# Kernel optimization log

Hardware: AMD Instinct MI355X
Metric: run time of the kernel (lower is better)

## Reference

```python
import jax, jax.numpy as jnp
import numpy as np

N_INST, N_PERS, N_PROD = 20000, 50000, 30000
E_INST, E_PERS, E_PROD = 160000, 400000, 240000
F_IN, HID, HEADS, OUT = 128, 64, 4, 2
D = HID * HEADS  # 256
NEG_SLOPE_ATT = 0.2   # GATv2 attention leaky-relu slope
NEG_SLOPE_ACT = 0.01  # F.leaky_relu default
BN_EPS = 1e-5


def gatv2(x, src, dst, Wl, Wr, att, b, N):
    """Single-relation GATv2Conv (concat heads, add_self_loops=True)."""
    loop = jnp.arange(N, dtype=src.dtype)
    s = jnp.concatenate([src, loop])
    d = jnp.concatenate([dst, loop])
    H, C = att.shape
    hl = (x @ Wl).reshape(N, H, C)  # source transform
    hr = (x @ Wr).reshape(N, H, C)  # target transform
    e = jax.nn.leaky_relu(hl[s] + hr[d], NEG_SLOPE_ATT)        # [E,H,C]
    score = jnp.einsum('ehc,hc->eh', e, att)                   # [E,H]
    mx = jax.lax.stop_gradient(jax.ops.segment_max(score, d, num_segments=N))
    ex = jnp.exp(score - mx[d])
    den = jax.ops.segment_sum(ex, d, num_segments=N)           # [N,H]
    alpha = ex / (den[d] + 1e-16)
    out = jax.ops.segment_sum(alpha[..., None] * hl[s], d, num_segments=N)
    return out.reshape(N, H * C) + b


def batchnorm(x, g, b):
    mu = jnp.mean(x, axis=0)
    var = jnp.var(x, axis=0)
    return (x - mu) * jax.lax.rsqrt(var + BN_EPS) * g + b


def setup_inputs() -> dict:
    key = jax.random.key(0)
    ks = jax.random.split(key, 16)
    s = 0.05
    return {
        'x_inst': jax.random.normal(ks[0], (N_INST, F_IN), jnp.float32),
        'x_pers': jax.random.normal(ks[1], (N_PERS, F_IN), jnp.float32),
        'x_prod': jax.random.normal(ks[2], (N_PROD, F_IN), jnp.float32),
        'ei_inst': jax.random.randint(ks[3], (2, E_INST), 0, N_INST, jnp.int32),
        'ei_pers': jax.random.randint(ks[4], (2, E_PERS), 0, N_PERS, jnp.int32),
        'ei_prod': jax.random.randint(ks[5], (2, E_PROD), 0, N_PROD, jnp.int32),
        'Wl1': jax.random.normal(ks[6], (3, F_IN, D), jnp.float32) * s,
        'Wr1': jax.random.normal(ks[7], (3, F_IN, D), jnp.float32) * s,
        'att1': jax.random.normal(ks[8], (3, HEADS, HID), jnp.float32) * s,
        'b1': jnp.zeros((3, D), jnp.float32),
        'Wl2': jax.random.normal(ks[9], (3, D, D), jnp.float32) * s,
        'Wr2': jax.random.normal(ks[10], (3, D, D), jnp.float32) * s,
        'att2': jax.random.normal(ks[11], (3, HEADS, HID), jnp.float32) * s,
        'b2': jnp.zeros((3, D), jnp.float32),
        'bn_g': jnp.ones((3, D), jnp.float32),
        'bn_b': jnp.zeros((3, D), jnp.float32),
        'cW': jax.random.normal(ks[12], (D, OUT), jnp.float32) * s,
        'cb': jnp.zeros((OUT,), jnp.float32),
    }


def reference(x_inst, x_pers, x_prod, ei_inst, ei_pers, ei_prod,
              Wl1, Wr1, att1, b1, Wl2, Wr2, att2, b2,
              bn_g, bn_b, cW, cb):
    xs = (x_inst, x_pers, x_prod)
    eis = (ei_inst, ei_pers, ei_prod)
    outs = []
    for i in range(3):  # fixed set of node types
        x = xs[i]
        N = x.shape[0]
        src, dst = eis[i][0], eis[i][1]
        h = gatv2(x, src, dst, Wl1[i], Wr1[i], att1[i], b1[i], N)
        h = jax.nn.leaky_relu(batchnorm(h, bn_g[i], bn_b[i]), NEG_SLOPE_ACT)
        h = gatv2(h, src, dst, Wl2[i], Wr2[i], att2[i], b2[i], N)
        h = jax.nn.leaky_relu(batchnorm(h, bn_g[i], bn_b[i]), NEG_SLOPE_ACT)
        outs.append(h @ cW + cb)
    return tuple(outs)
```

## Files before the change

### kernel.cpp

```cpp
#include <hip/hip_runtime.h>

#define DFEAT 256
#define NEG_ATT 0.2f
#define NEG_ACT 0.01f
#define BN_EPS 1e-5f

typedef short bf16x8 __attribute__((ext_vector_type(8)));
typedef float f32x4 __attribute__((ext_vector_type(4)));

struct Int3 { int a[3]; };
struct Cp3 { const void* p[3]; };
struct Vp3 { void* p[3]; };
struct WJobs { const float* src[12]; unsigned short* dst[12]; int K[12]; };

__device__ __forceinline__ float lrelu(float x, float s) { return x > 0.f ? x : s * x; }

__device__ __forceinline__ unsigned short f2bf(float f) {
    union { float f; unsigned int u; } v; v.f = f;
    unsigned int u = v.u;
    unsigned int r = (u + 0x7FFFu + ((u >> 16) & 1u)) >> 16;
    return (unsigned short)r;
}
__device__ __forceinline__ float bf2f(unsigned short s) {
    union { unsigned int u; float f; } v; v.u = ((unsigned int)s) << 16;
    return v.f;
}
__device__ __forceinline__ float u_lo(unsigned u) {
    union { unsigned u; float f; } v; v.u = u << 16; return v.f;
}
__device__ __forceinline__ float u_hi(unsigned u) {
    union { unsigned u; float f; } v; v.u = u & 0xffff0000u; return v.f;
}

__global__ __launch_bounds__(256)
void hist_all_k(Cp3 dst, Int3 E, int* __restrict__ counts_all, Int3 nodeOff) {
    int t = blockIdx.y;
    int e = blockIdx.x * 256 + threadIdx.x;
    if (e >= E.a[t]) return;
    const int* dstp = (const int*)dst.p[t];
    atomicAdd(&counts_all[nodeOff.a[t] + dstp[e]], 1);
}

__global__ __launch_bounds__(256)
void scan1_all_k(const int* __restrict__ counts_all, int* __restrict__ offs_all,
                 int* __restrict__ bsums_all, Int3 N, Int3 nodeOff, Int3 bOff) {
    int t = blockIdx.y;
    if (blockIdx.x * 256 >= N.a[t]) return;
    const int* counts = counts_all + nodeOff.a[t];
    int* offs = offs_all + nodeOff.a[t] + t;
    int* bsums = bsums_all + bOff.a[t];
    __shared__ int buf[256];
    int tt = threadIdx.x;
    int i = blockIdx.x * 256 + tt;
    int v = (i < N.a[t]) ? counts[i] : 0;
    buf[tt] = v;
    __syncthreads();
    for (int off = 1; off < 256; off <<= 1) {
        int x = (tt >= off) ? buf[tt - off] : 0;
        __syncthreads();
        buf[tt] += x;
        __syncthreads();
    }
    if (i < N.a[t]) offs[i] = buf[tt];
    if (tt == 255) bsums[blockIdx.x] = buf[255];
}

__global__ __launch_bounds__(256)
void scan2_all_k(int* __restrict__ bsums_all, Int3 N, Int3 bOff) {
    int t = blockIdx.x;
    int nb = (N.a[t] + 255) / 256;
    int* bsums = bsums_all + bOff.a[t];
    __shared__ int buf[256];
    __shared__ int carry_s;
    int tt = threadIdx.x;
    if (tt == 0) carry_s = 0;
    __syncthreads();
    for (int base = 0; base < nb; base += 256) {
        int i = base + tt;
        int v = (i < nb) ? bsums[i] : 0;
        buf[tt] = v;
        __syncthreads();
        for (int off = 1; off < 256; off <<= 1) {
            int x = (tt >= off) ? buf[tt - off] : 0;
            __syncthreads();
            buf[tt] += x;
            __syncthreads();
        }
        int incl = buf[tt];
        int c = carry_s;
        if (i < nb) bsums[i] = c + incl - v;
        __syncthreads();
        if (tt == 255) carry_s = c + buf[255];
        __syncthreads();
    }
}

__global__ __launch_bounds__(256)
void scan3_all_k(int* __restrict__ offs_all, const int* __restrict__ counts_all,
                 const int* __restrict__ bsums_all, Int3 N, Int3 E,
                 Int3 nodeOff, Int3 bOff) {
    int t = blockIdx.y;
    if (blockIdx.x * 256 >= N.a[t]) return;
    int* offs = offs_all + nodeOff.a[t] + t;
    const int* counts = counts_all + nodeOff.a[t];
    const int* bsums = bsums_all + bOff.a[t];
    int i = blockIdx.x * 256 + threadIdx.x;
    if (i < N.a[t]) offs[i] = offs[i] - counts[i] + bsums[blockIdx.x];
    if (i == 0) offs[N.a[t]] = E.a[t];
}

__global__ __launch_bounds__(256)
void scatter_all_k(Cp3 src, Cp3 dst, Int3 E, const int* __restrict__ offs_all,
                   int* __restrict__ counts_all, int* __restrict__ csr_all,
                   Int3 nodeOff, Int3 edgeOff) {
    int t = blockIdx.y;
    int e = blockIdx.x * 256 + threadIdx.x;
    if (e >= E.a[t]) return;
    const int* srcp = (const int*)src.p[t];
    const int* dstp = (const int*)dst.p[t];
    const int* offs = offs_all + nodeOff.a[t] + t;
    int* cursor = counts_all + nodeOff.a[t];
    int* csr = csr_all + edgeOff.a[t];
    int d = dstp[e];
    int pos = atomicSub(&cursor[d], 1) - 1;
    csr[offs[d] + pos] = srcp[e];
}

__global__ __launch_bounds__(256)
void wcast_tr_k(WJobs jobs) {
    int j = blockIdx.z;
    int K = jobs.K[j];
    int k0 = blockIdx.y * 64;
    if (k0 >= K) return;
    int n0 = blockIdx.x * 64;
    const float* W = jobs.src[j];
    unsigned short* Bt = jobs.dst[j];
    __shared__ float tile[64][65];
    int tid = threadIdx.x;
    int tr = tid >> 4;
    int tc4 = (tid & 15) << 2;
#pragma unroll
    for (int r = 0; r < 4; ++r) {
        int k = tr + r * 16;
        float4 v = *(const float4*)(W + (size_t)(k0 + k) * 256 + n0 + tc4);
        tile[k][tc4] = v.x; tile[k][tc4 + 1] = v.y;
        tile[k][tc4 + 2] = v.z; tile[k][tc4 + 3] = v.w;
    }
    __syncthreads();
    int n = tid >> 2;
    int kc = (tid & 3) << 4;
    unsigned o[8];
#pragma unroll
    for (int q = 0; q < 8; ++q) {
        float v0 = tile[kc + 2 * q][n];
        float v1 = tile[kc + 2 * q + 1][n];
        o[q] = (unsigned)f2bf(v0) | ((unsigned)f2bf(v1) << 16);
    }
    unsigned short* dp = Bt + (size_t)(n0 + n) * K + k0 + kc;
    *(uint4*)dp = make_uint4(o[0], o[1], o[2], o[3]);
    *(uint4*)(dp + 8) = make_uint4(o[4], o[5], o[6], o[7]);
}

template<int AMODE>
__global__ __launch_bounds__(256)
void mfma_gemm_all_k(Cp3 Ap3, Cp3 Bp3, Cp3 ssP, Vp3 Cp3v, Int3 M3, int K) {
    int t = blockIdx.z;
    int M = M3.a[t];
    int bm = blockIdx.x * 128;
    if (bm >= M) return;
    const void* Ap = Ap3.p[t];
    const unsigned short* Bt = (const unsigned short*)Bp3.p[t];
    const float* ss = (const float*)ssP.p[t];
    unsigned short* C = (unsigned short*)Cp3v.p[t];
    const int LDK = 40;
    __shared__ unsigned short As[128 * LDK];
    __shared__ unsigned short Bs[128 * LDK];
    int tid = threadIdx.x;
    int bn = blockIdx.y * 128;
    int wid = tid >> 6, lane = tid & 63;
    int quad = lane >> 4, l16 = lane & 15;
    int mw = (wid & 1) * 64, nw = (wid >> 1) * 64;
    f32x4 acc[4][4] = {};
    for (int k0 = 0; k0 < K; k0 += 32) {
#pragma unroll
        for (int i = 0; i < 2; ++i) {
            int c = tid + 256 * i;
            int row = c >> 2, ko = (c & 3) * 8;
            int ra = bm + row; if (ra >= M) ra = M - 1;
            if (AMODE == 1) {
                const float* Af = (const float*)Ap;
                float4 a0 = *(const float4*)(Af + (size_t)ra * K + k0 + ko);
                float4 a1 = *(const float4*)(Af + (size_t)ra * K + k0 + ko + 4);
                ushort4 lo, hi;
                lo.x = f2bf(a0.x); lo.y = f2bf(a0.y); lo.z = f2bf(a0.z); lo.w = f2bf(a0.w);
                hi.x = f2bf(a1.x); hi.y = f2bf(a1.y); hi.z = f2bf(a1.z); hi.w = f2bf(a1.w);
                *(ushort4*)&As[row * LDK + ko] = lo;
                *(ushort4*)&As[row * LDK + ko + 4] = hi;
            } else if (AMODE == 2) {
                const unsigned short* Ab = (const unsigned short*)Ap;
                uint4 va = *(const uint4*)(Ab + (size_t)ra * K + k0 + ko);
                const unsigned* up = (const unsigned*)&va;
                float4 sc0 = *(const float4*)(ss + k0 + ko);
                float4 sc1 = *(const float4*)(ss + k0 + ko + 4);
                float4 sh0 = *(const float4*)(ss + 256 + k0 + ko);
                float4 sh1 = *(const float4*)(ss + 256 + k0 + ko + 4);
                float fv[8] = {u_lo(up[0]), u_hi(up[0]), u_lo(up[1]), u_hi(up[1]),
                               u_lo(up[2]), u_hi(up[2]), u_lo(up[3]), u_hi(up[3])};
                float scv[8] = {sc0.x, sc0.y, sc0.z, sc0.w, sc1.x, sc1.y, sc1.z, sc1.w};
                float shv[8] = {sh0.x, sh0.y, sh0.z, sh0.w, sh1.x, sh1.y, sh1.z, sh1.w};
                unsigned ov[4];
#pragma unroll
                for (int q = 0; q < 4; ++q) {
                    float v0 = fmaf(fv[2 * q], scv[2 * q], shv[2 * q]);
                    v0 = fmaxf(v0, NEG_ACT * v0);
                    float v1 = fmaf(fv[2 * q + 1], scv[2 * q + 1], shv[2 * q + 1]);
                    v1 = fmaxf(v1, NEG_ACT * v1);
                    ov[q] = (unsigned)f2bf(v0) | ((unsigned)f2bf(v1) << 16);
                }
                *(uint4*)&As[row * LDK + ko] = make_uint4(ov[0], ov[1], ov[2], ov[3]);
            } else {
                const unsigned short* Ab = (const unsigned short*)Ap;
                uint4 va = *(const uint4*)(Ab + (size_t)ra * K + k0 + ko);
                *(uint4*)&As[row * LDK + ko] = va;
            }
            uint4 vb = *(const uint4*)(Bt + (size_t)(bn + row) * K + k0 + ko);
            *(uint4*)&Bs[row * LDK + ko] = vb;
        }
        __syncthreads();
        bf16x8 af[4], bfv[4];
#pragma unroll
        for (int i = 0; i < 4; ++i)
            af[i] = *(bf16x8*)&As[(mw + 16 * i + l16) * LDK + quad * 8];
#pragma unroll
        for (int u = 0; u < 4; ++u)
            bfv[u] = *(bf16x8*)&Bs[(nw + 16 * u + l16) * LDK + quad * 8];
#pragma unroll
        for (int i = 0; i < 4; ++i)
#pragma unroll
            for (int u = 0; u < 4; ++u)
                acc[i][u] = __builtin_amdgcn_mfma_f32_16x16x32_bf16(af[i], bfv[u], acc[i][u], 0, 0, 0);
        __syncthreads();
    }
#pragma unroll
    for (int i = 0; i < 4; ++i) {
#pragma unroll
        for (int r = 0; r < 4; ++r) {
            int grow = bm + mw + 16 * i + quad * 4 + r;
            if (grow < M) {
#pragma unroll
                for (int u = 0; u < 4; ++u) {
                    int gcol = bn + nw + 16 * u + l16;
                    C[(size_t)grow * 512 + gcol] = f2bf(acc[i][u][r]);
                }
            }
        }
    }
}

__global__ __launch_bounds__(256)
void gat_gather_all_k(Cp3 hl3, Cp3 offs3, Cp3 csr3, Cp3 att3, Cp3 bias3,
                      Vp3 out3, Int3 N3) {
    int t = blockIdx.z;
    int N = N3.a[t];
    int wave = (blockIdx.x * 256 + threadIdx.x) >> 6;
    int lane = threadIdx.x & 63;
    if (wave >= N) return;
    const char* hlB = (const char*)hl3.p[t];
    const int* offs = (const int*)offs3.p[t];
    const int* csr = (const int*)csr3.p[t];
    const float* att = (const float*)att3.p[t];
    const float* bias = (const float*)bias3.p[t];
    unsigned short* out = (unsigned short*)out3.p[t];
    int d = wave;
    unsigned lOff = (unsigned)lane << 3;
    ushort4 hru = *(const ushort4*)(hlB + (((unsigned)d << 10) + 512u + lOff));
    float hr0 = bf2f(hru.x), hr1 = bf2f(hru.y), hr2 = bf2f(hru.z), hr3 = bf2f(hru.w);
    float4 av  = *(const float4*)(att + (lane << 2));
    float4 bv  = *(const float4*)(bias + (lane << 2));
    float l = 0.f, ac0 = 0.f, ac1 = 0.f, ac2 = 0.f, ac3 = 0.f;

    auto update = [&](ushort4 u) {
        float h0 = bf2f(u.x), h1 = bf2f(u.y), h2 = bf2f(u.z), h3 = bf2f(u.w);
        float x0 = h0 + hr0; x0 = fmaxf(x0, NEG_ATT * x0);
        float x1 = h1 + hr1; x1 = fmaxf(x1, NEG_ATT * x1);
        float x2 = h2 + hr2; x2 = fmaxf(x2, NEG_ATT * x2);
        float x3 = h3 + hr3; x3 = fmaxf(x3, NEG_ATT * x3);
        float part = x0 * av.x;
        part = fmaf(x1, av.y, part);
        part = fmaf(x2, av.z, part);
        part = fmaf(x3, av.w, part);
        part += __shfl_xor(part, 1);
        part += __shfl_xor(part, 2);
        part += __shfl_xor(part, 4);
        part += __shfl_xor(part, 8);
        float p = __expf(part);
        l += p;
        ac0 = fmaf(p, h0, ac0); ac1 = fmaf(p, h1, ac1);
        ac2 = fmaf(p, h2, ac2); ac3 = fmaf(p, h3, ac3);
    };

    update(*(const ushort4*)(hlB + (((unsigned)d << 10) + lOff)));

    int beg = offs[d];
    int deg = offs[d + 1] - beg;
    for (int base = 0; base < deg; base += 64) {
        int cnt = min(64, deg - base);
        int my = (base + lane < deg) ? csr[beg + base + lane] : d;
        for (int j = 0; j < cnt; j += 8) {
            int kk = min(8, cnt - j);
            ushort4 v[8];
#pragma unroll
            for (int u = 0; u < 8; ++u) {
                int s = __shfl(my, (j + u) & 63);
                if (u < kk) v[u] = *(const ushort4*)(hlB + (((unsigned)s << 10) + lOff));
            }
#pragma unroll
            for (int u = 0; u < 8; ++u)
                if (u < kk) update(v[u]);
        }
    }
    float inv = 1.f / (l + 1e-16f);
    ushort4 o;
    o.x = f2bf(fmaf(ac0, inv, bv.x));
    o.y = f2bf(fmaf(ac1, inv, bv.y));
    o.z = f2bf(fmaf(ac2, inv, bv.z));
    o.w = f2bf(fmaf(ac3, inv, bv.w));
    *(ushort4*)((char*)out + (((unsigned)d << 9) + lOff)) = o;
}

__global__ __launch_bounds__(256)
void bn_stats_all_k(Cp3 h3, Vp3 st3, Int3 N3) {
    int t = blockIdx.y;
    const unsigned short* hp = (const unsigned short*)h3.p[t];
    float* st = (float*)st3.p[t];
    long total = (long)N3.a[t] * 256;
    int tid = threadIdx.x;
    long gt = (long)blockIdx.x * 256 + tid;
    long stride = (long)gridDim.x * 256 * 8;
    float s[8] = {0.f}, s2[8] = {0.f};
    for (long p = gt * 8; p < total; p += stride) {
        uint4 u = *(const uint4*)(hp + p);
        unsigned short* us = (unsigned short*)&u;
#pragma unroll
        for (int j = 0; j < 8; ++j) { float v = bf2f(us[j]); s[j] += v; s2[j] += v * v; }
    }
#pragma unroll
    for (int j = 0; j < 8; ++j) { s[j] += __shfl_xor(s[j], 32); s2[j] += __shfl_xor(s2[j], 32); }
    __shared__ float lds[2048];
    int wv = tid >> 6, lane = tid & 63;
    if (lane < 32) {
#pragma unroll
        for (int j = 0; j < 8; ++j) {
            lds[wv * 512 + lane * 8 + j] = s[j];
            lds[wv * 512 + 256 + lane * 8 + j] = s2[j];
        }
    }
    __syncthreads();
    for (int q = tid; q < 512; q += 256) {
        float v = lds[q] + lds[512 + q] + lds[1024 + q] + lds[1536 + q];
        atomicAdd(&st[q], v);
    }
}

__global__ __launch_bounds__(256)
void bn_finalize_all_k(Cp3 st3, const float* __restrict__ gb, const float* __restrict__ bb,
                       Vp3 ss3, Int3 N3) {
    int t = blockIdx.x;
    const float* st = (const float*)st3.p[t];
    float* ss = (float*)ss3.p[t];
    int f = threadIdx.x;
    float invN = 1.f / (float)N3.a[t];
    float mu  = st[f] * invN;
    float var = st[256 + f] * invN - mu * mu;
    float sc  = gb[t * DFEAT + f] / sqrtf(var + BN_EPS);
    ss[f] = sc;
    ss[256 + f] = bb[t * DFEAT + f] - mu * sc;
}

__global__ __launch_bounds__(256)
void bn_cls_all_k(Cp3 R3, Cp3 st3, const float* __restrict__ gb, const float* __restrict__ bb,
                  const float* __restrict__ cW, const float* __restrict__ cb,
                  Vp3 out3, Int3 N3) {
    int t = blockIdx.y;
    int N = N3.a[t];
    int wave = (blockIdx.x * 256 + threadIdx.x) >> 6;
    int lane = threadIdx.x & 63;
    if (wave >= N) return;
    const unsigned short* R = (const unsigned short*)R3.p[t];
    const float* stats = (const float*)st3.p[t];
    const float* g = gb + (size_t)t * DFEAT;
    const float* b = bb + (size_t)t * DFEAT;
    float* out = (float*)out3.p[t];
    int f4 = lane << 2;
    float invN = 1.f / (float)N;
    ushort4 u = *(const ushort4*)(R + (size_t)wave * DFEAT + f4);
    float vv[4] = {bf2f(u.x), bf2f(u.y), bf2f(u.z), bf2f(u.w)};
    float p0 = 0.f, p1 = 0.f;
#pragma unroll
    for (int j = 0; j < 4; ++j) {
        int f = f4 + j;
        float mu  = stats[f] * invN;
        float var = stats[DFEAT + f] * invN - mu * mu;
        float sc  = g[f] / sqrtf(var + BN_EPS);
        float val = lrelu((vv[j] - mu) * sc + b[f], NEG_ACT);
        float2 w = *(const float2*)(cW + (size_t)f * 2);
        p0 += val * w.x;
        p1 += val * w.y;
    }
#pragma unroll
    for (int off = 1; off < 64; off <<= 1) {
        p0 += __shfl_xor(p0, off);
        p1 += __shfl_xor(p1, off);
    }
    if (lane == 0) {
        out[(size_t)wave * 2 + 0] = p0 + cb[0];
        out[(size_t)wave * 2 + 1] = p1 + cb[1];
    }
}

extern "C" void kernel_launch(void* const* d_in, const int* in_sizes, int n_in,
                              void* d_out, int out_size, void* d_ws, size_t ws_size,
                              hipStream_t stream) {
    const float* x0 = (const float*)d_in[0];
    const float* x1 = (const float*)d_in[1];
    const float* x2 = (const float*)d_in[2];
    const int* ei[3] = {(const int*)d_in[3], (const int*)d_in[4], (const int*)d_in[5]};
    const float* Wl1 = (const float*)d_in[6];
    const float* Wr1 = (const float*)d_in[7];
    const float* att1 = (const float*)d_in[8];
    const float* b1 = (const float*)d_in[9];
    const float* Wl2 = (const float*)d_in[10];
    const float* Wr2 = (const float*)d_in[11];
    const float* att2 = (const float*)d_in[12];
    const float* b2 = (const float*)d_in[13];
    const float* bn_g = (const float*)d_in[14];
    const float* bn_b = (const float*)d_in[15];
    const float* cW = (const float*)d_in[16];
    const float* cb = (const float*)d_in[17];

    Int3 N3, E3, nodeOff, edgeOff, bOff;
    N3.a[0] = in_sizes[0] / 128; N3.a[1] = in_sizes[1] / 128; N3.a[2] = in_sizes[2] / 128;
    E3.a[0] = in_sizes[3] / 2;   E3.a[1] = in_sizes[4] / 2;   E3.a[2] = in_sizes[5] / 2;
    int Ntot = 0, Etot = 0, btot = 0;
    int maxN = 0, maxE = 0;
    for (int i = 0; i < 3; ++i) {
        nodeOff.a[i] = Ntot; edgeOff.a[i] = Etot; bOff.a[i] = btot;
        Ntot += N3.a[i]; Etot += E3.a[i]; btot += (N3.a[i] + 255) / 256;
        if (N3.a[i] > maxN) maxN = N3.a[i];
        if (E3.a[i] > maxE) maxE = E3.a[i];
    }

    char* w = (char*)d_ws;
    auto alloc_b = [&](size_t bytes) -> void* {
        void* p = (void*)w;
        w += (bytes + 255) & ~(size_t)255;
        return p;
    };
    unsigned short* C_all  = (unsigned short*)alloc_b((size_t)Ntot * 512 * sizeof(unsigned short));
    unsigned short* Rb_all = (unsigned short*)alloc_b((size_t)Ntot * DFEAT * sizeof(unsigned short));
    unsigned short* Bt1 = (unsigned short*)alloc_b((size_t)3 * 512 * 128 * sizeof(unsigned short));
    unsigned short* Bt2 = (unsigned short*)alloc_b((size_t)3 * 512 * 256 * sizeof(unsigned short));
    int* counts_all = (int*)alloc_b((size_t)Ntot * sizeof(int));
    int* offs_all   = (int*)alloc_b((size_t)(Ntot + 3) * sizeof(int));
    int* csr_all    = (int*)alloc_b((size_t)Etot * sizeof(int));
    int* bsums_all  = (int*)alloc_b((size_t)btot * sizeof(int));
    float* stats_all = (float*)alloc_b((size_t)6 * 512 * sizeof(float));
    float* ss_all    = (float*)alloc_b((size_t)3 * 512 * sizeof(float));

    Cp3 srcP, dstP, xP, Bt1P, Bt2P, hlP, offsP, csrP, att1P, att2P, b1P, b2P;
    Cp3 RbCP, st1CP, st2CP, ssCP, dumP;
    Vp3 CP, RbP, st1P, st2P, ssP, outP;
    for (int i = 0; i < 3; ++i) {
        srcP.p[i] = ei[i];
        dstP.p[i] = ei[i] + E3.a[i];
        xP.p[i] = (i == 0) ? (const void*)x0 : (i == 1) ? (const void*)x1 : (const void*)x2;
        Bt1P.p[i] = Bt1 + (size_t)i * 512 * 128;
        Bt2P.p[i] = Bt2 + (size_t)i * 512 * 256;
        CP.p[i] = C_all + (size_t)nodeOff.a[i] * 512;
        hlP.p[i] = CP.p[i];
        RbP.p[i] = Rb_all + (size_t)nodeOff.a[i] * DFEAT;
        RbCP.p[i] = RbP.p[i];
        offsP.p[i] = offs_all + nodeOff.a[i] + i;
        csrP.p[i] = csr_all + edgeOff.a[i];
        att1P.p[i] = att1 + (size_t)i * DFEAT;
        att2P.p[i] = att2 + (size_t)i * DFEAT;
        b1P.p[i] = b1 + (size_t)i * DFEAT;
        b2P.p[i] = b2 + (size_t)i * DFEAT;
        st1P.p[i] = stats_all + (size_t)i * 512;
        st2P.p[i] = stats_all + (size_t)(3 + i) * 512;
        st1CP.p[i] = st1P.p[i];
        st2CP.p[i] = st2P.p[i];
        ssP.p[i] = ss_all + (size_t)i * 512;
        ssCP.p[i] = ssP.p[i];
        dumP.p[i] = xP.p[i];
        outP.p[i] = (float*)d_out + (size_t)nodeOff.a[i] * 2;
    }

    int maxNblk = (maxN + 255) / 256;
    int maxEblk = (maxE + 255) / 256;
    int maxMtile = (maxN + 127) / 128;
    int maxNwave = (maxN + 3) / 4;

    hipMemsetAsync(counts_all, 0, (size_t)Ntot * sizeof(int), stream);
    hipMemsetAsync(stats_all, 0, (size_t)6 * 512 * sizeof(float), stream);
    {
        WJobs jobs;
        for (int i = 0; i < 3; ++i) {
            jobs.src[i * 4 + 0] = Wl1 + (size_t)i * 128 * 256;
            jobs.dst[i * 4 + 0] = (unsigned short*)Bt1P.p[i];
            jobs.K[i * 4 + 0] = 128;
            jobs.src[i * 4 + 1] = Wr1 + (size_t)i * 128 * 256;
            jobs.dst[i * 4 + 1] = (unsigned short*)Bt1P.p[i] + (size_t)256 * 128;
            jobs.K[i * 4 + 1] = 128;
            jobs.src[i * 4 + 2] = Wl2 + (size_t)i * 256 * 256;
            jobs.dst[i * 4 + 2] = (unsigned short*)Bt2P.p[i];
            jobs.K[i * 4 + 2] = 256;
            jobs.src[i * 4 + 3] = Wr2 + (size_t)i * 256 * 256;
            jobs.dst[i * 4 + 3] = (unsigned short*)Bt2P.p[i] + (size_t)256 * 256;
            jobs.K[i * 4 + 3] = 256;
        }
        wcast_tr_k<<<dim3(4, 4, 12), 256, 0, stream>>>(jobs);
    }

    hist_all_k<<<dim3(maxEblk, 3), 256, 0, stream>>>(dstP, E3, counts_all, nodeOff);
    scan1_all_k<<<dim3(maxNblk, 3), 256, 0, stream>>>(counts_all, offs_all, bsums_all, N3, nodeOff, bOff);
    scan2_all_k<<<3, 256, 0, stream>>>(bsums_all, N3, bOff);
    scan3_all_k<<<dim3(maxNblk, 3), 256, 0, stream>>>(offs_all, counts_all, bsums_all, N3, E3, nodeOff, bOff);
    scatter_all_k<<<dim3(maxEblk, 3), 256, 0, stream>>>(srcP, dstP, E3, offs_all, counts_all, csr_all, nodeOff, edgeOff);

    mfma_gemm_all_k<1><<<dim3(maxMtile, 4, 3), 256, 0, stream>>>(xP, Bt1P, dumP, CP, N3, 128);
    gat_gather_all_k<<<dim3(maxNwave, 1, 3), 256, 0, stream>>>(hlP, offsP, csrP, att1P, b1P, RbP, N3);
    bn_stats_all_k<<<dim3(512, 3), 256, 0, stream>>>(RbCP, st1P, N3);
    bn_finalize_all_k<<<3, 256, 0, stream>>>(st1CP, bn_g, bn_b, ssP, N3);

    mfma_gemm_all_k<2><<<dim3(maxMtile, 4, 3), 256, 0, stream>>>(RbCP, Bt2P, ssCP, CP, N3, 256);
    gat_gather_all_k<<<dim3(maxNwave, 1, 3), 256, 0, stream>>>(hlP, offsP, csrP, att2P, b2P, RbP, N3);
    bn_stats_all_k<<<dim3(512, 3), 256, 0, stream>>>(RbCP, st2P, N3);

    bn_cls_all_k<<<dim3(maxNwave, 3), 256, 0, stream>>>(RbCP, st2CP, bn_g, bn_b, cW, cb, outP, N3);
}
```

Measured before the change: 562.2 us.

## Fuse three-pass CSR scan into one block-per-type kernel and fold memsets into wcast

```diff
diff --git a/kernel.cpp b/kernel.cpp
--- a/kernel.cpp
+++ b/kernel.cpp
@@ -41,72 +41,63 @@
     atomicAdd(&counts_all[nodeOff.a[t] + dstp[e]], 1);
 }
 
-__global__ __launch_bounds__(256)
-void scan1_all_k(const int* __restrict__ counts_all, int* __restrict__ offs_all,
-                 int* __restrict__ bsums_all, Int3 N, Int3 nodeOff, Int3 bOff) {
-    int t = blockIdx.y;
-    if (blockIdx.x * 256 >= N.a[t]) return;
+__global__ __launch_bounds__(1024)
+void scan_fused_k(const int* __restrict__ counts_all, int* __restrict__ offs_all,
+                  Int3 N3, Int3 E3, Int3 nodeOff) {
+    int t = blockIdx.x;
+    int N = N3.a[t];
     const int* counts = counts_all + nodeOff.a[t];
     int* offs = offs_all + nodeOff.a[t] + t;
-    int* bsums = bsums_all + bOff.a[t];
-    __shared__ int buf[256];
-    int tt = threadIdx.x;
-    int i = blockIdx.x * 256 + tt;
-    int v = (i < N.a[t]) ? counts[i] : 0;
-    buf[tt] = v;
-    __syncthreads();
-    for (int off = 1; off < 256; off <<= 1) {
-        int x = (tt >= off) ? buf[tt - off] : 0;
+    __shared__ int ldsT[16];
+    __shared__ int ldsE[16];
+    __shared__ int ldsTot;
+    int tid = threadIdx.x;
+    int wv = tid >> 6, lane = tid & 63;
+    int carry = 0;
+    for (int base = 0; base < N; base += 8192) {
+        int idx0 = base + tid * 8;
+        int c[8];
+#pragma unroll
+        for (int j = 0; j < 8; ++j) {
+            int i = idx0 + j;
+            c[j] = (i < N) ? counts[i] : 0;
+        }
+        int tsum = 0;
+#pragma unroll
+        for (int j = 0; j < 8; ++j) tsum += c[j];
+        int incl = tsum;
+#pragma unroll
+        for (int off = 1; off < 64; off <<= 1) {
+            int v = __shfl_up(incl, off);
+            if (lane >= off) incl += v;
+        }
+        int texcl = incl - tsum;
+        if (lane == 63) ldsT[wv] = incl;
         __syncthreads();
-        buf[tt] += x;
+        if (wv == 0) {
+            int v = (lane < 16) ? ldsT[lane] : 0;
+            int inc2 = v;
+#pragma unroll
+            for (int off = 1; off < 16; off <<= 1) {
+                int u2 = __shfl_up(inc2, off);
+                if (lane >= off) inc2 += u2;
+            }
+            if (lane < 16) ldsE[lane] = inc2 - v;
+            if (lane == 15) ldsTot = inc2;
+        }
         __syncthreads();
-    }
-    if (i < N.a[t]) offs[i] = buf[tt];
-    if (tt == 255) bsums[blockIdx.x] = buf[255];
-}
-
-__global__ __launch_bounds__(256)
-void scan2_all_k(int* __restrict__ bsums_all, Int3 N, Int3 bOff) {
-    int t = blockIdx.x;
-    int nb = (N.a[t] + 255) / 256;
-    int* bsums = bsums_all + bOff.a[t];
-    __shared__ int buf[256];
-    __shared__ int carry_s;
-    int tt = threadIdx.x;
-    if (tt == 0) carry_s = 0;
-    __syncthreads();
-    for (int base = 0; base < nb; base += 256) {
-        int i = base + tt;
-        int v = (i < nb) ? bsums[i] : 0;
-        buf[tt] = v;
+        int mybase = carry + ldsE[wv] + texcl;
+        int pfx = 0;
+#pragma unroll
+        for (int j = 0; j < 8; ++j) {
+            int i = idx0 + j;
+            if (i < N) offs[i] = mybase + pfx;
+            pfx += c[j];
+        }
+        carry += ldsTot;
         __syncthreads();
-        for (int off = 1; off < 256; off <<= 1) {
-            int x = (tt >= off) ? buf[tt - off] : 0;
-            __syncthreads();
-            buf[tt] += x;
-            __syncthreads();
-        }
-        int incl = buf[tt];
-        int c = carry_s;
-        if (i < nb) bsums[i] = c + incl - v;
-        __syncthreads();
-        if (tt == 255) carry_s = c + buf[255];
-        __syncthreads();
-    }
-}
-
-__global__ __launch_bounds__(256)
-void scan3_all_k(int* __restrict__ offs_all, const int* __restrict__ counts_all,
-                 const int* __restrict__ bsums_all, Int3 N, Int3 E,
-                 Int3 nodeOff, Int3 bOff) {
-    int t = blockIdx.y;
-    if (blockIdx.x * 256 >= N.a[t]) return;
-    int* offs = offs_all + nodeOff.a[t] + t;
-    const int* counts = counts_all + nodeOff.a[t];
-    const int* bsums = bsums_all + bOff.a[t];
-    int i = blockIdx.x * 256 + threadIdx.x;
-    if (i < N.a[t]) offs[i] = offs[i] - counts[i] + bsums[blockIdx.x];
-    if (i == 0) offs[N.a[t]] = E.a[t];
+    }
+    if (tid == 0) offs[N] = E3.a[t];
 }
 
 __global__ __launch_bounds__(256)
@@ -127,7 +118,15 @@
 }
 
 __global__ __launch_bounds__(256)
-void wcast_tr_k(WJobs jobs) {
+void wcast_tr_k(WJobs jobs, int* __restrict__ counts_all, int Ntot,
+                float* __restrict__ stats_all) {
+    {
+        int bid = (blockIdx.z * gridDim.y + blockIdx.y) * gridDim.x + blockIdx.x;
+        int nthr = gridDim.x * gridDim.y * gridDim.z * 256;
+        int gtid = bid * 256 + threadIdx.x;
+        for (int i = gtid; i < Ntot; i += nthr) counts_all[i] = 0;
+        for (int i = gtid; i < 3072; i += nthr) stats_all[i] = 0.f;
+    }
     int j = blockIdx.z;
     int K = jobs.K[j];
     int k0 = blockIdx.y * 64;
@@ -438,14 +437,14 @@
     const float* cW = (const float*)d_in[16];
     const float* cb = (const float*)d_in[17];
 
-    Int3 N3, E3, nodeOff, edgeOff, bOff;
+    Int3 N3, E3, nodeOff, edgeOff;
     N3.a[0] = in_sizes[0] / 128; N3.a[1] = in_sizes[1] / 128; N3.a[2] = in_sizes[2] / 128;
     E3.a[0] = in_sizes[3] / 2;   E3.a[1] = in_sizes[4] / 2;   E3.a[2] = in_sizes[5] / 2;
-    int Ntot = 0, Etot = 0, btot = 0;
+    int Ntot = 0, Etot = 0;
     int maxN = 0, maxE = 0;
     for (int i = 0; i < 3; ++i) {
-        nodeOff.a[i] = Ntot; edgeOff.a[i] = Etot; bOff.a[i] = btot;
-        Ntot += N3.a[i]; Etot += E3.a[i]; btot += (N3.a[i] + 255) / 256;
+        nodeOff.a[i] = Ntot; edgeOff.a[i] = Etot;
+        Ntot += N3.a[i]; Etot += E3.a[i];
         if (N3.a[i] > maxN) maxN = N3.a[i];
         if (E3.a[i] > maxE) maxE = E3.a[i];
     }
@@ -463,7 +462,6 @@
     int* counts_all = (int*)alloc_b((size_t)Ntot * sizeof(int));
     int* offs_all   = (int*)alloc_b((size_t)(Ntot + 3) * sizeof(int));
     int* csr_all    = (int*)alloc_b((size_t)Etot * sizeof(int));
-    int* bsums_all  = (int*)alloc_b((size_t)btot * sizeof(int));
     float* stats_all = (float*)alloc_b((size_t)6 * 512 * sizeof(float));
     float* ss_all    = (float*)alloc_b((size_t)3 * 512 * sizeof(float));
 
@@ -496,13 +494,10 @@
         outP.p[i] = (float*)d_out + (size_t)nodeOff.a[i] * 2;
     }
 
-    int maxNblk = (maxN + 255) / 256;
     int maxEblk = (maxE + 255) / 256;
     int maxMtile = (maxN + 127) / 128;
     int maxNwave = (maxN + 3) / 4;
 
-    hipMemsetAsync(counts_all, 0, (size_t)Ntot * sizeof(int), stream);
-    hipMemsetAsync(stats_all, 0, (size_t)6 * 512 * sizeof(float), stream);
     {
         WJobs jobs;
         for (int i = 0; i < 3; ++i) {
@@ -519,13 +514,11 @@
             jobs.dst[i * 4 + 3] = (unsigned short*)Bt2P.p[i] + (size_t)256 * 256;
             jobs.K[i * 4 + 3] = 256;
         }
-        wcast_tr_k<<<dim3(4, 4, 12), 256, 0, stream>>>(jobs);
+        wcast_tr_k<<<dim3(4, 4, 12), 256, 0, stream>>>(jobs, counts_all, Ntot, stats_all);
     }
 
     hist_all_k<<<dim3(maxEblk, 3), 256, 0, stream>>>(dstP, E3, counts_all, nodeOff);
-    scan1_all_k<<<dim3(maxNblk, 3), 256, 0, stream>>>(counts_all, offs_all, bsums_all, N3, nodeOff, bOff);
-    scan2_all_k<<<3, 256, 0, stream>>>(bsums_all, N3, bOff);
-    scan3_all_k<<<dim3(maxNblk, 3), 256, 0, stream>>>(offs_all, counts_all, bsums_all, N3, E3, nodeOff, bOff);
+    scan_fused_k<<<3, 1024, 0, stream>>>(counts_all, offs_all, N3, E3, nodeOff);
     scatter_all_k<<<dim3(maxEblk, 3), 256, 0, stream>>>(srcP, dstP, E3, offs_all, counts_all, csr_all, nodeOff, edgeOff);
 
     mfma_gemm_all_k<1><<<dim3(maxMtile, 4, 3), 256, 0, stream>>>(xP, Bt1P, dumP, CP, N3, 128);
```

Measured after the change: 593.9 us. 5.6% more time.
